# Kernel optimization log

Measured on AMD Instinct MI355X. Metric: run time of the kernel, lower is better.

The kernel has to match this reference:

```python
import jax, jax.numpy as jnp
import numpy as np

D_MODEL = 1024
N_HEADS = 16
D_K = D_MODEL // N_HEADS


def setup_inputs() -> dict:
    key = jax.random.key(0)
    ks = jax.random.split(key, 12)
    B, S, D = 4, 2048, D_MODEL
    scale = 1.0 / np.sqrt(D)
    inp = {
        'query': jax.random.normal(ks[0], (B, S, D), jnp.float32),
        'key': jax.random.normal(ks[1], (B, S, D), jnp.float32),
        'value': jax.random.normal(ks[2], (B, S, D), jnp.float32),
        'Wq': jax.random.normal(ks[3], (D, D), jnp.float32) * scale,
        'bq': jax.random.normal(ks[4], (D,), jnp.float32) * 0.02,
        'Wk': jax.random.normal(ks[5], (D, D), jnp.float32) * scale,
        'bk': jax.random.normal(ks[6], (D,), jnp.float32) * 0.02,
        'Wv': jax.random.normal(ks[7], (D, D), jnp.float32) * scale,
        'bv': jax.random.normal(ks[8], (D,), jnp.float32) * 0.02,
        'Wo': jax.random.normal(ks[9], (D, D), jnp.float32) * scale,
        'bo': jax.random.normal(ks[10], (D,), jnp.float32) * 0.02,
    }
    return inp


def reference(query, key, value, Wq, bq, Wk, bk, Wv, bv, Wo, bo):
    B, S, D = query.shape
    # torch nn.Linear: y = x @ W^T + b
    def proj(x, W, b):
        y = jnp.einsum('bsd,ed->bse', x, W) + b
        # [B,S,D] -> [B,H,S,d_k]
        return y.reshape(B, S, N_HEADS, D_K).transpose(0, 2, 1, 3)

    q = proj(query, Wq, bq)
    k = proj(key, Wk, bk)
    v = proj(value, Wv, bv)

    scores = jnp.einsum('bhqd,bhkd->bhqk', q, k) / jnp.sqrt(jnp.float32(D_K))
    attn = jax.nn.softmax(scores, axis=-1)  # dropout = identity (eval mode)
    out = jnp.einsum('bhqk,bhkd->bhqd', attn, v)
    out = out.transpose(0, 2, 1, 3).reshape(B, S, D)
    return jnp.einsum('bsd,ed->bse', out, Wo) + bo
```

## Files before the change

kernel.cpp:

```cpp
#include <hip/hip_runtime.h>
#include <hip/hip_bf16.h>
#include <cstdint>
#include <cstddef>


#define BATCH   4
#define SEQ     2048
#define D_MODEL 1024
#define NHEADS  16
#define DK      64

typedef __attribute__((ext_vector_type(8))) __bf16 bf16x8_t;
typedef __attribute__((ext_vector_type(4))) float  f32x4;

__device__ inline unsigned int pack2(float lo, float hi) {
  __hip_bfloat162 h = __float22bfloat162_rn(make_float2(lo, hi));
  union { __hip_bfloat162 h; unsigned int u; } c; c.h = h; return c.u;
}
__device__ inline unsigned short f2bf(float f) { return (unsigned short)pack2(f, f); }

#if __has_builtin(__builtin_amdgcn_exp2f)
__device__ inline float fexp2(float x) { return __builtin_amdgcn_exp2f(x); }
#else
__device__ inline float fexp2(float x) { return __expf(x * 0.6931471805599453f); }
#endif

__device__ inline void cvt8(const float* __restrict__ s, unsigned short* __restrict__ d) {
  const float4 a = *(const float4*)s;
  const float4 b = *(const float4*)(s + 4);
  uint4 r;
  r.x = pack2(a.x, a.y); r.y = pack2(a.z, a.w);
  r.z = pack2(b.x, b.y); r.w = pack2(b.z, b.w);
  *(uint4*)d = r;
}

typedef __attribute__((address_space(3))) unsigned int lds_u32_t;
typedef const __attribute__((address_space(1))) unsigned int glb_u32_t;
__device__ inline void gld16(const unsigned short* g, unsigned short* l) {
  __builtin_amdgcn_global_load_lds((glb_u32_t*)(uintptr_t)g,
                                   (lds_u32_t*)(unsigned int)(uintptr_t)l, 16, 0, 0);
}

__global__ __launch_bounds__(256) void cvt3_kernel(
    const float* __restrict__ a, const float* __restrict__ b, const float* __restrict__ c,
    unsigned short* __restrict__ oa, unsigned short* __restrict__ ob, unsigned short* __restrict__ oc)
{
  const float* s = (blockIdx.y == 0) ? a : (blockIdx.y == 1) ? b : c;
  unsigned short* d = (blockIdx.y == 0) ? oa : (blockIdx.y == 1) ? ob : oc;
  const size_t i = ((size_t)blockIdx.x * 256 + threadIdx.x) * 8;
  cvt8(s + i, d + i);
}
__global__ __launch_bounds__(256) void cvt4_kernel(
    const float* __restrict__ a, const float* __restrict__ b,
    const float* __restrict__ c, const float* __restrict__ dd,
    unsigned short* __restrict__ oa, unsigned short* __restrict__ ob,
    unsigned short* __restrict__ oc, unsigned short* __restrict__ od)
{
  const float* s = (blockIdx.y == 0) ? a : (blockIdx.y == 1) ? b : (blockIdx.y == 2) ? c : dd;
  unsigned short* d = (blockIdx.y == 0) ? oa : (blockIdx.y == 1) ? ob : (blockIdx.y == 2) ? oc : od;
  const size_t i = ((size_t)blockIdx.x * 256 + threadIdx.x) * 8;
  cvt8(s + i, d + i);
}

__device__ inline void gemm_core(const unsigned short* __restrict__ A,
                                 const unsigned short* __restrict__ W,
                                 unsigned short* a_lds, unsigned short* b_lds,
                                 int m0, int n0, f32x4 (&acc)[4][4])
{
  const int tid  = threadIdx.x;
  const int lane = tid & 63;
  const int wv   = tid >> 6;
  const int l15  = lane & 15;
  const int quad = lane >> 4;
  const int wm = (wv & 1) * 64;
  const int wn = (wv >> 1) * 64;

  const int srow = tid >> 2;
  const int sch  = (tid & 3) ^ (srow & 3);
  const unsigned short* Ap0 = A + (size_t)(m0 + srow) * D_MODEL + sch * 8;
  const unsigned short* Ap1 = Ap0 + (size_t)64 * D_MODEL;
  const unsigned short* Wp0 = W + (size_t)(n0 + srow) * D_MODEL + sch * 8;
  const unsigned short* Wp1 = Wp0 + (size_t)64 * D_MODEL;
  unsigned short* al0 = a_lds + wv * 512;
  unsigned short* al1 = a_lds + 2048 + wv * 512;
  unsigned short* bl0 = b_lds + wv * 512;
  unsigned short* bl1 = b_lds + 2048 + wv * 512;

  const int pq = (quad ^ (l15 & 3)) * 8;

  for (int k0 = 0; k0 < D_MODEL; k0 += 32) {
    __syncthreads();
    gld16(Ap0 + k0, al0);
    gld16(Ap1 + k0, al1);
    gld16(Wp0 + k0, bl0);
    gld16(Wp1 + k0, bl1);
    __syncthreads();

    bf16x8_t af[4], bfr[4];
#pragma unroll
    for (int i = 0; i < 4; ++i)
      af[i] = *(const bf16x8_t*)&a_lds[(wm + i * 16 + l15) * 32 + pq];
#pragma unroll
    for (int j = 0; j < 4; ++j)
      bfr[j] = *(const bf16x8_t*)&b_lds[(wn + j * 16 + l15) * 32 + pq];

#pragma unroll
    for (int i = 0; i < 4; ++i)
#pragma unroll
      for (int j = 0; j < 4; ++j)
        acc[i][j] = __builtin_amdgcn_mfma_f32_16x16x32_bf16(af[i], bfr[j], acc[i][j], 0, 0, 0);
  }
}

__global__ __launch_bounds__(256) void qkv_kernel(
    const unsigned short* __restrict__ qb, const unsigned short* __restrict__ kb,
    const unsigned short* __restrict__ vb,
    const unsigned short* __restrict__ wq, const unsigned short* __restrict__ wk,
    const unsigned short* __restrict__ wvp,
    const float* __restrict__ bq, const float* __restrict__ bk, const float* __restrict__ bv,
    unsigned short* __restrict__ Qws, unsigned short* __restrict__ Kws,
    unsigned short* __restrict__ Vws)
{
  __shared__ unsigned short a_lds[128 * 32];
  __shared__ unsigned short b_lds[128 * 32];

  const int z = blockIdx.z;
  const unsigned short* A = (z == 0) ? qb : (z == 1) ? kb : vb;
  const unsigned short* W = (z == 0) ? wq : (z == 1) ? wk : wvp;
  const float* bias       = (z == 0) ? bq : (z == 1) ? bk : bv;
  unsigned short* C       = (z == 0) ? Qws : (z == 1) ? Kws : Vws;
  const int m0 = blockIdx.x * 128;
  const int n0 = blockIdx.y * 128;

  f32x4 acc[4][4];
#pragma unroll
  for (int i = 0; i < 4; ++i)
#pragma unroll
    for (int j = 0; j < 4; ++j)
      acc[i][j] = (f32x4){0.f, 0.f, 0.f, 0.f};

  gemm_core(A, W, a_lds, b_lds, m0, n0, acc);

  const int tid  = threadIdx.x;
  const int lane = tid & 63;
  const int wv   = tid >> 6;
  const int l15  = lane & 15;
  const int quad = lane >> 4;
  const int wm = (wv & 1) * 64;
  const int wn = (wv >> 1) * 64;
  if (z == 2) {
    for (int j = 0; j < 4; ++j) {
      const int n = n0 + wn + j * 16 + l15;
      const int hh = n >> 6, dd = n & 63;
      const float bvl = bias[n];
      for (int i = 0; i < 4; ++i) {
        const int mbase = m0 + wm + i * 16 + quad * 4;
        const int bb = mbase >> 11, ss = mbase & 2047;
        uint2 w2 = make_uint2(pack2(acc[i][j][0] + bvl, acc[i][j][1] + bvl),
                              pack2(acc[i][j][2] + bvl, acc[i][j][3] + bvl));
        *(uint2*)(C + (((size_t)bb * NHEADS + hh) * DK + dd) * SEQ + ss) = w2;
      }
    }
  } else {
    const float oscale = (z == 0) ? 0.18033688011112042f : 1.0f;
    for (int j = 0; j < 4; ++j) {
      const int n = n0 + wn + j * 16 + l15;
      const int hh = n >> 6, dd = n & 63;
      const float bvl = bias[n];
      for (int i = 0; i < 4; ++i) {
        const int mbase = m0 + wm + i * 16 + quad * 4;
        const int bb = mbase >> 11, ss = mbase & 2047;
        unsigned short* dst = C + (((size_t)bb * NHEADS + hh) * SEQ + ss) * DK + dd;
        for (int r = 0; r < 4; ++r)
          dst[(size_t)r * DK] = f2bf((acc[i][j][r] + bvl) * oscale);
      }
    }
  }
}

__global__ __launch_bounds__(256) void outproj_kernel(
    const unsigned short* __restrict__ A, const unsigned short* __restrict__ W,
    const float* __restrict__ bias, float* __restrict__ C)
{
  __shared__ unsigned short a_lds[128 * 32];
  __shared__ unsigned short b_lds[128 * 32];
  const int m0 = blockIdx.x * 128;
  const int n0 = blockIdx.y * 128;

  f32x4 acc[4][4];
#pragma unroll
  for (int i = 0; i < 4; ++i)
#pragma unroll
    for (int j = 0; j < 4; ++j)
      acc[i][j] = (f32x4){0.f, 0.f, 0.f, 0.f};

  gemm_core(A, W, a_lds, b_lds, m0, n0, acc);

  const int tid  = threadIdx.x;
  const int lane = tid & 63;
  const int wv   = tid >> 6;
  const int l15  = lane & 15;
  const int quad = lane >> 4;
  const int wm = (wv & 1) * 64;
  const int wn = (wv >> 1) * 64;
  for (int j = 0; j < 4; ++j) {
    const int n = n0 + wn + j * 16 + l15;
    const float bvl = bias[n];
    for (int i = 0; i < 4; ++i) {
      const int mbase = m0 + wm + i * 16 + quad * 4;
      for (int r = 0; r < 4; ++r)
        C[(size_t)(mbase + r) * D_MODEL + n] = acc[i][j][r] + bvl;
    }
  }
}

__global__ __launch_bounds__(512, 6) void attn_kernel(
    const unsigned short* __restrict__ Q,
    const unsigned short* __restrict__ K,
    const unsigned short* __restrict__ Vt,
    unsigned short* __restrict__ Oattn)
{
  __shared__ unsigned short k_sw[2 * 64 * 64];
  __shared__ unsigned short vt_sw[2 * 64 * 64];

  const int tid  = threadIdx.x;
  const int lane = tid & 63;
  const int wv   = tid >> 6;
  const int l15  = lane & 15;
  const int quad = lane >> 4;
  const int bh   = blockIdx.x;
  const int q0   = blockIdx.y * 128;
  const size_t hoff = (size_t)bh * SEQ * DK;
  const unsigned short* Qh  = Q  + hoff;
  const unsigned short* Kh  = K  + hoff;
  const unsigned short* Vth = Vt + hoff;

  bf16x8_t qf0, qf1;
  {
    const unsigned short* qr = Qh + (size_t)(q0 + wv * 16 + l15) * DK;
    qf0 = *(const bf16x8_t*)(qr + quad * 8);
    qf1 = *(const bf16x8_t*)(qr + 32 + quad * 8);
  }

  f32x4 o[4];
#pragma unroll
  for (int t = 0; t < 4; ++t) o[t] = (f32x4){0.f, 0.f, 0.f, 0.f};
  float mval = -1e30f, lval = 0.f;

  const int sr  = lane >> 3;
  const int pc  = lane & 7;
  const int row = wv * 8 + sr;
  const int sem = pc ^ sr ^ wv;
  const unsigned short* KsA = Kh  + (size_t)row * DK  + sem * 8;
  const unsigned short* VsA = Vth + (size_t)row * SEQ + sem * 8;
  unsigned short* kd = k_sw  + wv * 512;
  unsigned short* vd = vt_sw + wv * 512;

#define STAGE(buf, key0) do {                                        \
    gld16(KsA + (size_t)(key0) * DK, kd + (buf) * 4096);             \
    gld16(VsA + (key0),              vd + (buf) * 4096);             \
  } while (0)

  const int srcA = l15 + ((quad & 1) << 5);
  const int srcB = srcA + 16;
  const int hi   = quad >> 1;

  STAGE(0, 0);
  __syncthreads();

  int cur = 0;
  for (int kb = 0; kb < SEQ / 64; ++kb) {
    if (kb + 1 < SEQ / 64) STAGE(cur ^ 1, (kb + 1) * 64);

    const unsigned short* kcur = k_sw  + cur * 4096;
    const unsigned short* vcur = vt_sw + cur * 4096;

    f32x4 s[4];
    __builtin_amdgcn_s_setprio(1);
#pragma unroll
    for (int t = 0; t < 4; ++t) {
      const int r = t * 16 + l15;
      const int sw = (r & 7) ^ (r >> 3);
      bf16x8_t kf0 = *(const bf16x8_t*)&kcur[r * 64 + ((quad ^ sw) << 3)];
      bf16x8_t kf1 = *(const bf16x8_t*)&kcur[r * 64 + (((quad | 4) ^ sw) << 3)];
      f32x4 z = (f32x4){0.f, 0.f, 0.f, 0.f};
      z = __builtin_amdgcn_mfma_f32_16x16x32_bf16(kf0, qf0, z, 0, 0, 0);
      z = __builtin_amdgcn_mfma_f32_16x16x32_bf16(kf1, qf1, z, 0, 0, 0);
      s[t] = z;
    }
    __builtin_amdgcn_s_setprio(0);

    float mx = s[0][0];
#pragma unroll
    for (int t = 0; t < 4; ++t)
#pragma unroll
      for (int r = 0; r < 4; ++r) mx = fmaxf(mx, s[t][r]);
    mx = fmaxf(mx, __shfl_xor(mx, 16));
    mx = fmaxf(mx, __shfl_xor(mx, 32));
    if (__any(mx > mval + 8.0f)) {
      const float mnew  = fmaxf(mval, mx);
      const float alpha = fexp2(mval - mnew);
      mval = mnew;
      lval *= alpha;
#pragma unroll
      for (int t = 0; t < 4; ++t) o[t] *= alpha;
    }
    float rs = 0.f;
    unsigned int u[4][2];
#pragma unroll
    for (int t = 0; t < 4; ++t) {
      const float p0 = fexp2(s[t][0] - mval);
      const float p1 = fexp2(s[t][1] - mval);
      const float p2 = fexp2(s[t][2] - mval);
      const float p3 = fexp2(s[t][3] - mval);
      rs += (p0 + p1) + (p2 + p3);
      u[t][0] = pack2(p0, p1);
      u[t][1] = pack2(p2, p3);
    }
    rs += __shfl_xor(rs, 16);
    rs += __shfl_xor(rs, 32);
    lval += rs;

    unsigned int w0[4], w1[4];
#pragma unroll
    for (int c = 0; c < 2; ++c) {
      unsigned int* wc = c ? w1 : w0;
      const unsigned int uA0 = u[2 * c][0],     uA1 = u[2 * c][1];
      const unsigned int uB0 = u[2 * c + 1][0], uB1 = u[2 * c + 1][1];
      unsigned int a, b;
      a = (unsigned int)__shfl((int)uA0, srcA); b = (unsigned int)__shfl((int)uB0, srcA);
      wc[0] = hi ? b : a;
      a = (unsigned int)__shfl((int)uA1, srcA); b = (unsigned int)__shfl((int)uB1, srcA);
      wc[1] = hi ? b : a;
      a = (unsigned int)__shfl((int)uA0, srcB); b = (unsigned int)__shfl((int)uB0, srcB);
      wc[2] = hi ? b : a;
      a = (unsigned int)__shfl((int)uA1, srcB); b = (unsigned int)__shfl((int)uB1, srcB);
      wc[3] = hi ? b : a;
    }
    union Cv { unsigned int w[4]; bf16x8_t v; };
    Cv cv0, cv1;
    cv0.w[0] = w0[0]; cv0.w[1] = w0[1]; cv0.w[2] = w0[2]; cv0.w[3] = w0[3];
    cv1.w[0] = w1[0]; cv1.w[1] = w1[1]; cv1.w[2] = w1[2]; cv1.w[3] = w1[3];
    const bf16x8_t pf0 = cv0.v;
    const bf16x8_t pf1 = cv1.v;

    __builtin_amdgcn_s_setprio(1);
#pragma unroll
    for (int nt = 0; nt < 4; ++nt) {
      const int r = nt * 16 + l15;
      const int sw = (r & 7) ^ (r >> 3);
      bf16x8_t vf0 = *(const bf16x8_t*)&vcur[r * 64 + ((quad ^ sw) << 3)];
      bf16x8_t vf1 = *(const bf16x8_t*)&vcur[r * 64 + (((quad | 4) ^ sw) << 3)];
      o[nt] = __builtin_amdgcn_mfma_f32_16x16x32_bf16(vf0, pf0, o[nt], 0, 0, 0);
      o[nt] = __builtin_amdgcn_mfma_f32_16x16x32_bf16(vf1, pf1, o[nt], 0, 0, 0);
    }
    __builtin_amdgcn_s_setprio(0);

    __syncthreads();
    cur ^= 1;
  }
#undef STAGE

  const int bb = bh >> 4, hh = bh & 15;
  const float inv = 1.0f / lval;
  unsigned short* orow = Oattn + (size_t)(bb * SEQ + q0 + wv * 16 + l15) * D_MODEL + hh * DK + quad * 4;
#pragma unroll
  for (int nt = 0; nt < 4; ++nt) {
    f32x4 v = o[nt];
    *(uint2*)(orow + nt * 16) = make_uint2(pack2(v[0] * inv, v[1] * inv),
                                           pack2(v[2] * inv, v[3] * inv));
  }
}

extern "C" void kernel_launch(void* const* d_in, const int* in_sizes, int n_in,
                              void* d_out, int out_size, void* d_ws, size_t ws_size,
                              hipStream_t stream) {
  const float* query = (const float*)d_in[0];
  const float* key   = (const float*)d_in[1];
  const float* value = (const float*)d_in[2];
  const float* Wq    = (const float*)d_in[3];
  const float* bq    = (const float*)d_in[4];
  const float* Wk    = (const float*)d_in[5];
  const float* bk    = (const float*)d_in[6];
  const float* Wv    = (const float*)d_in[7];
  const float* bv    = (const float*)d_in[8];
  const float* Wo    = (const float*)d_in[9];
  const float* bo    = (const float*)d_in[10];

  const size_t E  = (size_t)BATCH * SEQ * D_MODEL;
  const size_t WE = (size_t)D_MODEL * D_MODEL;
  unsigned short* ws  = (unsigned short*)d_ws;
  unsigned short* Qws = ws;
  unsigned short* Kws = ws + E;
  unsigned short* Vws = ws + 2 * E;
  unsigned short* qb  = ws + 3 * E;
  unsigned short* kb  = ws + 4 * E;
  unsigned short* vb  = ws + 5 * E;
  unsigned short* wqb = ws + 6 * E;
  unsigned short* wkb = wqb + WE;
  unsigned short* wvb = wqb + 2 * WE;
  unsigned short* wob = wqb + 3 * WE;
  unsigned short* Aws = qb;

  cvt3_kernel<<<dim3(E / 2048, 3), 256, 0, stream>>>(query, key, value, qb, kb, vb);
  cvt4_kernel<<<dim3(WE / 2048, 4), 256, 0, stream>>>(Wq, Wk, Wv, Wo, wqb, wkb, wvb, wob);

  qkv_kernel<<<dim3(BATCH * SEQ / 128, D_MODEL / 128, 3), 256, 0, stream>>>(
      qb, kb, vb, wqb, wkb, wvb, bq, bk, bv, Qws, Kws, Vws);
  attn_kernel<<<dim3(BATCH * NHEADS, SEQ / 128), 512, 0, stream>>>(Qws, Kws, Vws, Aws);
  outproj_kernel<<<dim3(BATCH * SEQ / 128, D_MODEL / 128), 256, 0, stream>>>(
      Aws, wob, bo, (float*)d_out);
}
```

Before: 402.5 us.

## Process two query tiles per attention block to reuse K/V staging

Each attention block now handles 256 query rows instead of 128: every wave keeps two independent Q fragments, accumulators and softmax states, and reuses each K/V tile loaded into shared memory for both. This halves the K/V global loads and LDS fragment reads per query row. The cost is higher register pressure (launch bounds lowered from 6 to 4 waves per SIMD) and half as many blocks in the grid (512), which may reduce occupancy and the ability to hide latency.

```diff
diff --git a/kernel.cpp b/kernel.cpp
--- a/kernel.cpp
+++ b/kernel.cpp
@@ -214,7 +214,34 @@
   }
 }
 
-__global__ __launch_bounds__(512, 6) void attn_kernel(
+__device__ inline void exchP(const unsigned int (&u)[4][2], int srcA, int srcB, int hi,
+                             bf16x8_t& pf0, bf16x8_t& pf1)
+{
+  unsigned int w0[4], w1[4];
+#pragma unroll
+  for (int c = 0; c < 2; ++c) {
+    unsigned int* wc = c ? w1 : w0;
+    const unsigned int uA0 = u[2 * c][0],     uA1 = u[2 * c][1];
+    const unsigned int uB0 = u[2 * c + 1][0], uB1 = u[2 * c + 1][1];
+    unsigned int a, b;
+    a = (unsigned int)__shfl((int)uA0, srcA); b = (unsigned int)__shfl((int)uB0, srcA);
+    wc[0] = hi ? b : a;
+    a = (unsigned int)__shfl((int)uA1, srcA); b = (unsigned int)__shfl((int)uB1, srcA);
+    wc[1] = hi ? b : a;
+    a = (unsigned int)__shfl((int)uA0, srcB); b = (unsigned int)__shfl((int)uB0, srcB);
+    wc[2] = hi ? b : a;
+    a = (unsigned int)__shfl((int)uA1, srcB); b = (unsigned int)__shfl((int)uB1, srcB);
+    wc[3] = hi ? b : a;
+  }
+  union Cv { unsigned int w[4]; bf16x8_t v; };
+  Cv cv0, cv1;
+  cv0.w[0] = w0[0]; cv0.w[1] = w0[1]; cv0.w[2] = w0[2]; cv0.w[3] = w0[3];
+  cv1.w[0] = w1[0]; cv1.w[1] = w1[1]; cv1.w[2] = w1[2]; cv1.w[3] = w1[3];
+  pf0 = cv0.v;
+  pf1 = cv1.v;
+}
+
+__global__ __launch_bounds__(512, 4) void attn_kernel(
     const unsigned short* __restrict__ Q,
     const unsigned short* __restrict__ K,
     const unsigned short* __restrict__ Vt,
@@ -229,23 +256,30 @@
   const int l15  = lane & 15;
   const int quad = lane >> 4;
   const int bh   = blockIdx.x;
-  const int q0   = blockIdx.y * 128;
+  const int q0   = blockIdx.y * 256;
   const size_t hoff = (size_t)bh * SEQ * DK;
   const unsigned short* Qh  = Q  + hoff;
   const unsigned short* Kh  = K  + hoff;
   const unsigned short* Vth = Vt + hoff;
 
-  bf16x8_t qf0, qf1;
+  bf16x8_t qfA0, qfA1, qfB0, qfB1;
   {
-    const unsigned short* qr = Qh + (size_t)(q0 + wv * 16 + l15) * DK;
-    qf0 = *(const bf16x8_t*)(qr + quad * 8);
-    qf1 = *(const bf16x8_t*)(qr + 32 + quad * 8);
-  }
-
-  f32x4 o[4];
-#pragma unroll
-  for (int t = 0; t < 4; ++t) o[t] = (f32x4){0.f, 0.f, 0.f, 0.f};
-  float mval = -1e30f, lval = 0.f;
+    const unsigned short* qrA = Qh + (size_t)(q0 + wv * 16 + l15) * DK;
+    const unsigned short* qrB = qrA + (size_t)128 * DK;
+    qfA0 = *(const bf16x8_t*)(qrA + quad * 8);
+    qfA1 = *(const bf16x8_t*)(qrA + 32 + quad * 8);
+    qfB0 = *(const bf16x8_t*)(qrB + quad * 8);
+    qfB1 = *(const bf16x8_t*)(qrB + 32 + quad * 8);
+  }
+
+  f32x4 oA[4], oB[4];
+#pragma unroll
+  for (int t = 0; t < 4; ++t) {
+    oA[t] = (f32x4){0.f, 0.f, 0.f, 0.f};
+    oB[t] = (f32x4){0.f, 0.f, 0.f, 0.f};
+  }
+  float mA = -1e30f, lA = 0.f;
+  float mB = -1e30f, lB = 0.f;
 
   const int sr  = lane >> 3;
   const int pc  = lane & 7;
@@ -275,7 +309,7 @@
     const unsigned short* kcur = k_sw  + cur * 4096;
     const unsigned short* vcur = vt_sw + cur * 4096;
 
-    f32x4 s[4];
+    f32x4 sA[4], sB[4];
     __builtin_amdgcn_s_setprio(1);
 #pragma unroll
     for (int t = 0; t < 4; ++t) {
@@ -283,66 +317,84 @@
       const int sw = (r & 7) ^ (r >> 3);
       bf16x8_t kf0 = *(const bf16x8_t*)&kcur[r * 64 + ((quad ^ sw) << 3)];
       bf16x8_t kf1 = *(const bf16x8_t*)&kcur[r * 64 + (((quad | 4) ^ sw) << 3)];
-      f32x4 z = (f32x4){0.f, 0.f, 0.f, 0.f};
-      z = __builtin_amdgcn_mfma_f32_16x16x32_bf16(kf0, qf0, z, 0, 0, 0);
-      z = __builtin_amdgcn_mfma_f32_16x16x32_bf16(kf1, qf1, z, 0, 0, 0);
-      s[t] = z;
+      f32x4 zA = (f32x4){0.f, 0.f, 0.f, 0.f};
+      zA = __builtin_amdgcn_mfma_f32_16x16x32_bf16(kf0, qfA0, zA, 0, 0, 0);
+      zA = __builtin_amdgcn_mfma_f32_16x16x32_bf16(kf1, qfA1, zA, 0, 0, 0);
+      sA[t] = zA;
+      f32x4 zB = (f32x4){0.f, 0.f, 0.f, 0.f};
+      zB = __builtin_amdgcn_mfma_f32_16x16x32_bf16(kf0, qfB0, zB, 0, 0, 0);
+      zB = __builtin_amdgcn_mfma_f32_16x16x32_bf16(kf1, qfB1, zB, 0, 0, 0);
+      sB[t] = zB;
     }
     __builtin_amdgcn_s_setprio(0);
 
-    float mx = s[0][0];
-#pragma unroll
-    for (int t = 0; t < 4; ++t)
-#pragma unroll
-      for (int r = 0; r < 4; ++r) mx = fmaxf(mx, s[t][r]);
-    mx = fmaxf(mx, __shfl_xor(mx, 16));
-    mx = fmaxf(mx, __shfl_xor(mx, 32));
-    if (__any(mx > mval + 8.0f)) {
-      const float mnew  = fmaxf(mval, mx);
-      const float alpha = fexp2(mval - mnew);
-      mval = mnew;
-      lval *= alpha;
-#pragma unroll
-      for (int t = 0; t < 4; ++t) o[t] *= alpha;
-    }
-    float rs = 0.f;
-    unsigned int u[4][2];
-#pragma unroll
-    for (int t = 0; t < 4; ++t) {
-      const float p0 = fexp2(s[t][0] - mval);
-      const float p1 = fexp2(s[t][1] - mval);
-      const float p2 = fexp2(s[t][2] - mval);
-      const float p3 = fexp2(s[t][3] - mval);
-      rs += (p0 + p1) + (p2 + p3);
-      u[t][0] = pack2(p0, p1);
-      u[t][1] = pack2(p2, p3);
-    }
-    rs += __shfl_xor(rs, 16);
-    rs += __shfl_xor(rs, 32);
-    lval += rs;
-
-    unsigned int w0[4], w1[4];
-#pragma unroll
-    for (int c = 0; c < 2; ++c) {
-      unsigned int* wc = c ? w1 : w0;
-      const unsigned int uA0 = u[2 * c][0],     uA1 = u[2 * c][1];
-      const unsigned int uB0 = u[2 * c + 1][0], uB1 = u[2 * c + 1][1];
-      unsigned int a, b;
-      a = (unsigned int)__shfl((int)uA0, srcA); b = (unsigned int)__shfl((int)uB0, srcA);
-      wc[0] = hi ? b : a;
-      a = (unsigned int)__shfl((int)uA1, srcA); b = (unsigned int)__shfl((int)uB1, srcA);
-      wc[1] = hi ? b : a;
-      a = (unsigned int)__shfl((int)uA0, srcB); b = (unsigned int)__shfl((int)uB0, srcB);
-      wc[2] = hi ? b : a;
-      a = (unsigned int)__shfl((int)uA1, srcB); b = (unsigned int)__shfl((int)uB1, srcB);
-      wc[3] = hi ? b : a;
-    }
-    union Cv { unsigned int w[4]; bf16x8_t v; };
-    Cv cv0, cv1;
-    cv0.w[0] = w0[0]; cv0.w[1] = w0[1]; cv0.w[2] = w0[2]; cv0.w[3] = w0[3];
-    cv1.w[0] = w1[0]; cv1.w[1] = w1[1]; cv1.w[2] = w1[2]; cv1.w[3] = w1[3];
-    const bf16x8_t pf0 = cv0.v;
-    const bf16x8_t pf1 = cv1.v;
+    bf16x8_t pfA0, pfA1, pfB0, pfB1;
+    {
+      float mx = sA[0][0];
+#pragma unroll
+      for (int t = 0; t < 4; ++t)
+#pragma unroll
+        for (int r = 0; r < 4; ++r) mx = fmaxf(mx, sA[t][r]);
+      mx = fmaxf(mx, __shfl_xor(mx, 16));
+      mx = fmaxf(mx, __shfl_xor(mx, 32));
+      if (__any(mx > mA + 8.0f)) {
+        const float mnew  = fmaxf(mA, mx);
+        const float alpha = fexp2(mA - mnew);
+        mA = mnew;
+        lA *= alpha;
+#pragma unroll
+        for (int t = 0; t < 4; ++t) oA[t] *= alpha;
+      }
+      float rs = 0.f;
+      unsigned int u[4][2];
+#pragma unroll
+      for (int t = 0; t < 4; ++t) {
+        const float p0 = fexp2(sA[t][0] - mA);
+        const float p1 = fexp2(sA[t][1] - mA);
+        const float p2 = fexp2(sA[t][2] - mA);
+        const float p3 = fexp2(sA[t][3] - mA);
+        rs += (p0 + p1) + (p2 + p3);
+        u[t][0] = pack2(p0, p1);
+        u[t][1] = pack2(p2, p3);
+      }
+      rs += __shfl_xor(rs, 16);
+      rs += __shfl_xor(rs, 32);
+      lA += rs;
+      exchP(u, srcA, srcB, hi, pfA0, pfA1);
+    }
+    {
+      float mx = sB[0][0];
+#pragma unroll
+      for (int t = 0; t < 4; ++t)
+#pragma unroll
+        for (int r = 0; r < 4; ++r) mx = fmaxf(mx, sB[t][r]);
+      mx = fmaxf(mx, __shfl_xor(mx, 16));
+      mx = fmaxf(mx, __shfl_xor(mx, 32));
+      if (__any(mx > mB + 8.0f)) {
+        const float mnew  = fmaxf(mB, mx);
+        const float alpha = fexp2(mB - mnew);
+        mB = mnew;
+        lB *= alpha;
+#pragma unroll
+        for (int t = 0; t < 4; ++t) oB[t] *= alpha;
+      }
+      float rs = 0.f;
+      unsigned int u[4][2];
+#pragma unroll
+      for (int t = 0; t < 4; ++t) {
+        const float p0 = fexp2(sB[t][0] - mB);
+        const float p1 = fexp2(sB[t][1] - mB);
+        const float p2 = fexp2(sB[t][2] - mB);
+        const float p3 = fexp2(sB[t][3] - mB);
+        rs += (p0 + p1) + (p2 + p3);
+        u[t][0] = pack2(p0, p1);
+        u[t][1] = pack2(p2, p3);
+      }
+      rs += __shfl_xor(rs, 16);
+      rs += __shfl_xor(rs, 32);
+      lB += rs;
+      exchP(u, srcA, srcB, hi, pfB0, pfB1);
+    }
 
     __builtin_amdgcn_s_setprio(1);
 #pragma unroll
@@ -351,8 +403,10 @@
       const int sw = (r & 7) ^ (r >> 3);
       bf16x8_t vf0 = *(const bf16x8_t*)&vcur[r * 64 + ((quad ^ sw) << 3)];
       bf16x8_t vf1 = *(const bf16x8_t*)&vcur[r * 64 + (((quad | 4) ^ sw) << 3)];
-      o[nt] = __builtin_amdgcn_mfma_f32_16x16x32_bf16(vf0, pf0, o[nt], 0, 0, 0);
-      o[nt] = __builtin_amdgcn_mfma_f32_16x16x32_bf16(vf1, pf1, o[nt], 0, 0, 0);
+      oA[nt] = __builtin_amdgcn_mfma_f32_16x16x32_bf16(vf0, pfA0, oA[nt], 0, 0, 0);
+      oA[nt] = __builtin_amdgcn_mfma_f32_16x16x32_bf16(vf1, pfA1, oA[nt], 0, 0, 0);
+      oB[nt] = __builtin_amdgcn_mfma_f32_16x16x32_bf16(vf0, pfB0, oB[nt], 0, 0, 0);
+      oB[nt] = __builtin_amdgcn_mfma_f32_16x16x32_bf16(vf1, pfB1, oB[nt], 0, 0, 0);
     }
     __builtin_amdgcn_s_setprio(0);
 
@@ -362,13 +416,25 @@
 #undef STAGE
 
   const int bb = bh >> 4, hh = bh & 15;
-  const float inv = 1.0f / lval;
-  unsigned short* orow = Oattn + (size_t)(bb * SEQ + q0 + wv * 16 + l15) * D_MODEL + hh * DK + quad * 4;
-#pragma unroll
-  for (int nt = 0; nt < 4; ++nt) {
-    f32x4 v = o[nt];
-    *(uint2*)(orow + nt * 16) = make_uint2(pack2(v[0] * inv, v[1] * inv),
-                                           pack2(v[2] * inv, v[3] * inv));
+  {
+    const float inv = 1.0f / lA;
+    unsigned short* orow = Oattn + (size_t)(bb * SEQ + q0 + wv * 16 + l15) * D_MODEL + hh * DK + quad * 4;
+#pragma unroll
+    for (int nt = 0; nt < 4; ++nt) {
+      f32x4 v = oA[nt];
+      *(uint2*)(orow + nt * 16) = make_uint2(pack2(v[0] * inv, v[1] * inv),
+                                             pack2(v[2] * inv, v[3] * inv));
+    }
+  }
+  {
+    const float inv = 1.0f / lB;
+    unsigned short* orow = Oattn + (size_t)(bb * SEQ + q0 + 128 + wv * 16 + l15) * D_MODEL + hh * DK + quad * 4;
+#pragma unroll
+    for (int nt = 0; nt < 4; ++nt) {
+      f32x4 v = oB[nt];
+      *(uint2*)(orow + nt * 16) = make_uint2(pack2(v[0] * inv, v[1] * inv),
+                                             pack2(v[2] * inv, v[3] * inv));
+    }
   }
 }
 
@@ -407,7 +473,7 @@
 
   qkv_kernel<<<dim3(BATCH * SEQ / 128, D_MODEL / 128, 3), 256, 0, stream>>>(
       qb, kb, vb, wqb, wkb, wvb, bq, bk, bv, Qws, Kws, Vws);
-  attn_kernel<<<dim3(BATCH * NHEADS, SEQ / 128), 512, 0, stream>>>(Qws, Kws, Vws, Aws);
+  attn_kernel<<<dim3(BATCH * NHEADS, SEQ / 256), 512, 0, stream>>>(Qws, Kws, Vws, Aws);
   outproj_kernel<<<dim3(BATCH * SEQ / 128, D_MODEL / 128), 256, 0, stream>>>(
       Aws, wob, bo, (float*)d_out);
 }
```

After: 375.3 us. 1.07x faster.

## Switch attention to 32x32x16 MFMA with 32 query rows per wave

Applied to the files above, without the earlier changes.

Rewrites the attention inner loop to use 32x32x16 bf16 MFMA tiles, so each wave handles 32 query rows and each block 256, halving the grid's y dimension. The larger tile halves the number of blocks that reload each K/V tile through LDS. It also replaces the cross-lane shuffle that rebuilt the P operand with a single xor-32 exchange. In exchange, register pressure rises, so the launch-bounds occupancy hint drops from 6 to 4 and fewer waves are resident per CU.

```diff
diff --git a/kernel.cpp b/kernel.cpp
--- a/kernel.cpp
+++ b/kernel.cpp
@@ -10,8 +10,9 @@
 #define NHEADS  16
 #define DK      64
 
-typedef __attribute__((ext_vector_type(8))) __bf16 bf16x8_t;
-typedef __attribute__((ext_vector_type(4))) float  f32x4;
+typedef __attribute__((ext_vector_type(8)))  __bf16 bf16x8_t;
+typedef __attribute__((ext_vector_type(4)))  float  f32x4;
+typedef __attribute__((ext_vector_type(16))) float  f32x16;
 
 __device__ inline unsigned int pack2(float lo, float hi) {
   __hip_bfloat162 h = __float22bfloat162_rn(make_float2(lo, hi));
@@ -24,6 +25,10 @@
 #else
 __device__ inline float fexp2(float x) { return __expf(x * 0.6931471805599453f); }
 #endif
+
+__device__ inline unsigned int exch32(unsigned int x) {
+  return (unsigned int)__shfl_xor((int)x, 32);
+}
 
 __device__ inline void cvt8(const float* __restrict__ s, unsigned short* __restrict__ d) {
   const float4 a = *(const float4*)s;
@@ -214,7 +219,7 @@
   }
 }
 
-__global__ __launch_bounds__(512, 6) void attn_kernel(
+__global__ __launch_bounds__(512, 4) void attn_kernel(
     const unsigned short* __restrict__ Q,
     const unsigned short* __restrict__ K,
     const unsigned short* __restrict__ Vt,
@@ -226,25 +231,28 @@
   const int tid  = threadIdx.x;
   const int lane = tid & 63;
   const int wv   = tid >> 6;
-  const int l15  = lane & 15;
-  const int quad = lane >> 4;
+  const int l31  = lane & 31;
+  const int hb   = lane >> 5;
   const int bh   = blockIdx.x;
-  const int q0   = blockIdx.y * 128;
+  const int q0   = blockIdx.y * 256;
   const size_t hoff = (size_t)bh * SEQ * DK;
   const unsigned short* Qh  = Q  + hoff;
   const unsigned short* Kh  = K  + hoff;
   const unsigned short* Vth = Vt + hoff;
 
-  bf16x8_t qf0, qf1;
+  bf16x8_t qf[4];
   {
-    const unsigned short* qr = Qh + (size_t)(q0 + wv * 16 + l15) * DK;
-    qf0 = *(const bf16x8_t*)(qr + quad * 8);
-    qf1 = *(const bf16x8_t*)(qr + 32 + quad * 8);
+    const unsigned short* qr = Qh + (size_t)(q0 + wv * 32 + l31) * DK;
+#pragma unroll
+    for (int kk = 0; kk < 4; ++kk)
+      qf[kk] = *(const bf16x8_t*)(qr + kk * 16 + hb * 8);
   }
 
-  f32x4 o[4];
-#pragma unroll
-  for (int t = 0; t < 4; ++t) o[t] = (f32x4){0.f, 0.f, 0.f, 0.f};
+  f32x16 oAcc[2];
+#pragma unroll
+  for (int dh = 0; dh < 2; ++dh)
+#pragma unroll
+    for (int i = 0; i < 16; ++i) oAcc[dh][i] = 0.f;
   float mval = -1e30f, lval = 0.f;
 
   const int sr  = lane >> 3;
@@ -261,12 +269,11 @@
     gld16(VsA + (key0),              vd + (buf) * 4096);             \
   } while (0)
 
-  const int srcA = l15 + ((quad & 1) << 5);
-  const int srcB = srcA + 16;
-  const int hi   = quad >> 1;
-
   STAGE(0, 0);
   __syncthreads();
+
+  const int swr0 = (l31 & 7) ^ (l31 >> 3);
+  const int swr1 = (l31 & 7) ^ ((l31 >> 3) ^ 4);
 
   int cur = 0;
   for (int kb = 0; kb < SEQ / 64; ++kb) {
@@ -275,27 +282,33 @@
     const unsigned short* kcur = k_sw  + cur * 4096;
     const unsigned short* vcur = vt_sw + cur * 4096;
 
-    f32x4 s[4];
+    f32x16 s0, s1;
+#pragma unroll
+    for (int i = 0; i < 16; ++i) { s0[i] = 0.f; s1[i] = 0.f; }
     __builtin_amdgcn_s_setprio(1);
-#pragma unroll
-    for (int t = 0; t < 4; ++t) {
-      const int r = t * 16 + l15;
-      const int sw = (r & 7) ^ (r >> 3);
-      bf16x8_t kf0 = *(const bf16x8_t*)&kcur[r * 64 + ((quad ^ sw) << 3)];
-      bf16x8_t kf1 = *(const bf16x8_t*)&kcur[r * 64 + (((quad | 4) ^ sw) << 3)];
-      f32x4 z = (f32x4){0.f, 0.f, 0.f, 0.f};
-      z = __builtin_amdgcn_mfma_f32_16x16x32_bf16(kf0, qf0, z, 0, 0, 0);
-      z = __builtin_amdgcn_mfma_f32_16x16x32_bf16(kf1, qf1, z, 0, 0, 0);
-      s[t] = z;
+    {
+      const unsigned short* krow = kcur + l31 * 64;
+#pragma unroll
+      for (int kk = 0; kk < 4; ++kk) {
+        bf16x8_t kf = *(const bf16x8_t*)&krow[((2 * kk + hb) ^ swr0) << 3];
+        s0 = __builtin_amdgcn_mfma_f32_32x32x16_bf16(kf, qf[kk], s0, 0, 0, 0);
+      }
+    }
+    {
+      const unsigned short* krow = kcur + (32 + l31) * 64;
+#pragma unroll
+      for (int kk = 0; kk < 4; ++kk) {
+        bf16x8_t kf = *(const bf16x8_t*)&krow[((2 * kk + hb) ^ swr1) << 3];
+        s1 = __builtin_amdgcn_mfma_f32_32x32x16_bf16(kf, qf[kk], s1, 0, 0, 0);
+      }
     }
     __builtin_amdgcn_s_setprio(0);
 
-    float mx = s[0][0];
-#pragma unroll
-    for (int t = 0; t < 4; ++t)
-#pragma unroll
-      for (int r = 0; r < 4; ++r) mx = fmaxf(mx, s[t][r]);
-    mx = fmaxf(mx, __shfl_xor(mx, 16));
+    float mx = s0[0];
+#pragma unroll
+    for (int i = 1; i < 16; ++i) mx = fmaxf(mx, s0[i]);
+#pragma unroll
+    for (int i = 0; i < 16; ++i) mx = fmaxf(mx, s1[i]);
     mx = fmaxf(mx, __shfl_xor(mx, 32));
     if (__any(mx > mval + 8.0f)) {
       const float mnew  = fmaxf(mval, mx);
@@ -303,56 +316,80 @@
       mval = mnew;
       lval *= alpha;
 #pragma unroll
-      for (int t = 0; t < 4; ++t) o[t] *= alpha;
+      for (int dh = 0; dh < 2; ++dh)
+#pragma unroll
+        for (int i = 0; i < 16; ++i) oAcc[dh][i] *= alpha;
     }
     float rs = 0.f;
-    unsigned int u[4][2];
-#pragma unroll
-    for (int t = 0; t < 4; ++t) {
-      const float p0 = fexp2(s[t][0] - mval);
-      const float p1 = fexp2(s[t][1] - mval);
-      const float p2 = fexp2(s[t][2] - mval);
-      const float p3 = fexp2(s[t][3] - mval);
-      rs += (p0 + p1) + (p2 + p3);
-      u[t][0] = pack2(p0, p1);
-      u[t][1] = pack2(p2, p3);
-    }
-    rs += __shfl_xor(rs, 16);
+    unsigned int w0[8], w1[8];
+#pragma unroll
+    for (int m = 0; m < 8; ++m) {
+      const float p0 = fexp2(s0[2 * m] - mval);
+      const float p1 = fexp2(s0[2 * m + 1] - mval);
+      rs += p0 + p1;
+      w0[m] = pack2(p0, p1);
+    }
+#pragma unroll
+    for (int m = 0; m < 8; ++m) {
+      const float p0 = fexp2(s1[2 * m] - mval);
+      const float p1 = fexp2(s1[2 * m + 1] - mval);
+      rs += p0 + p1;
+      w1[m] = pack2(p0, p1);
+    }
     rs += __shfl_xor(rs, 32);
     lval += rs;
 
-    unsigned int w0[4], w1[4];
-#pragma unroll
-    for (int c = 0; c < 2; ++c) {
-      unsigned int* wc = c ? w1 : w0;
-      const unsigned int uA0 = u[2 * c][0],     uA1 = u[2 * c][1];
-      const unsigned int uB0 = u[2 * c + 1][0], uB1 = u[2 * c + 1][1];
-      unsigned int a, b;
-      a = (unsigned int)__shfl((int)uA0, srcA); b = (unsigned int)__shfl((int)uB0, srcA);
-      wc[0] = hi ? b : a;
-      a = (unsigned int)__shfl((int)uA1, srcA); b = (unsigned int)__shfl((int)uB1, srcA);
-      wc[1] = hi ? b : a;
-      a = (unsigned int)__shfl((int)uA0, srcB); b = (unsigned int)__shfl((int)uB0, srcB);
-      wc[2] = hi ? b : a;
-      a = (unsigned int)__shfl((int)uA1, srcB); b = (unsigned int)__shfl((int)uB1, srcB);
-      wc[3] = hi ? b : a;
-    }
     union Cv { unsigned int w[4]; bf16x8_t v; };
-    Cv cv0, cv1;
-    cv0.w[0] = w0[0]; cv0.w[1] = w0[1]; cv0.w[2] = w0[2]; cv0.w[3] = w0[3];
-    cv1.w[0] = w1[0]; cv1.w[1] = w1[1]; cv1.w[2] = w1[2]; cv1.w[3] = w1[3];
-    const bf16x8_t pf0 = cv0.v;
-    const bf16x8_t pf1 = cv1.v;
+    bf16x8_t pf[4];
+    {
+      const unsigned int e0 = exch32(w0[0]), e1 = exch32(w0[1]);
+      const unsigned int e2 = exch32(w0[2]), e3 = exch32(w0[3]);
+      Cv c;
+      c.w[0] = hb ? e2 : w0[0]; c.w[1] = hb ? e3 : w0[1];
+      c.w[2] = hb ? w0[2] : e0; c.w[3] = hb ? w0[3] : e1;
+      pf[0] = c.v;
+    }
+    {
+      const unsigned int e0 = exch32(w0[4]), e1 = exch32(w0[5]);
+      const unsigned int e2 = exch32(w0[6]), e3 = exch32(w0[7]);
+      Cv c;
+      c.w[0] = hb ? e2 : w0[4]; c.w[1] = hb ? e3 : w0[5];
+      c.w[2] = hb ? w0[6] : e0; c.w[3] = hb ? w0[7] : e1;
+      pf[1] = c.v;
+    }
+    {
+      const unsigned int e0 = exch32(w1[0]), e1 = exch32(w1[1]);
+      const unsigned int e2 = exch32(w1[2]), e3 = exch32(w1[3]);
+      Cv c;
+      c.w[0] = hb ? e2 : w1[0]; c.w[1] = hb ? e3 : w1[1];
+      c.w[2] = hb ? w1[2] : e0; c.w[3] = hb ? w1[3] : e1;
+      pf[2] = c.v;
+    }
+    {
+      const unsigned int e0 = exch32(w1[4]), e1 = exch32(w1[5]);
+      const unsigned int e2 = exch32(w1[6]), e3 = exch32(w1[7]);
+      Cv c;
+      c.w[0] = hb ? e2 : w1[4]; c.w[1] = hb ? e3 : w1[5];
+      c.w[2] = hb ? w1[6] : e0; c.w[3] = hb ? w1[7] : e1;
+      pf[3] = c.v;
+    }
 
     __builtin_amdgcn_s_setprio(1);
-#pragma unroll
-    for (int nt = 0; nt < 4; ++nt) {
-      const int r = nt * 16 + l15;
-      const int sw = (r & 7) ^ (r >> 3);
-      bf16x8_t vf0 = *(const bf16x8_t*)&vcur[r * 64 + ((quad ^ sw) << 3)];
-      bf16x8_t vf1 = *(const bf16x8_t*)&vcur[r * 64 + (((quad | 4) ^ sw) << 3)];
-      o[nt] = __builtin_amdgcn_mfma_f32_16x16x32_bf16(vf0, pf0, o[nt], 0, 0, 0);
-      o[nt] = __builtin_amdgcn_mfma_f32_16x16x32_bf16(vf1, pf1, o[nt], 0, 0, 0);
+    {
+      const unsigned short* vrow = vcur + l31 * 64;
+#pragma unroll
+      for (int t = 0; t < 4; ++t) {
+        bf16x8_t vf = *(const bf16x8_t*)&vrow[((2 * t + hb) ^ swr0) << 3];
+        oAcc[0] = __builtin_amdgcn_mfma_f32_32x32x16_bf16(vf, pf[t], oAcc[0], 0, 0, 0);
+      }
+    }
+    {
+      const unsigned short* vrow = vcur + (32 + l31) * 64;
+#pragma unroll
+      for (int t = 0; t < 4; ++t) {
+        bf16x8_t vf = *(const bf16x8_t*)&vrow[((2 * t + hb) ^ swr1) << 3];
+        oAcc[1] = __builtin_amdgcn_mfma_f32_32x32x16_bf16(vf, pf[t], oAcc[1], 0, 0, 0);
+      }
     }
     __builtin_amdgcn_s_setprio(0);
 
@@ -363,13 +400,18 @@
 
   const int bb = bh >> 4, hh = bh & 15;
   const float inv = 1.0f / lval;
-  unsigned short* orow = Oattn + (size_t)(bb * SEQ + q0 + wv * 16 + l15) * D_MODEL + hh * DK + quad * 4;
-#pragma unroll
-  for (int nt = 0; nt < 4; ++nt) {
-    f32x4 v = o[nt];
-    *(uint2*)(orow + nt * 16) = make_uint2(pack2(v[0] * inv, v[1] * inv),
-                                           pack2(v[2] * inv, v[3] * inv));
-  }
+  unsigned short* orow = Oattn + (size_t)(bb * SEQ + q0 + wv * 32 + l31) * D_MODEL
+                       + hh * DK + hb * 4;
+#pragma unroll
+  for (int dh = 0; dh < 2; ++dh)
+#pragma unroll
+    for (int a = 0; a < 4; ++a) {
+      const float v0 = oAcc[dh][4 * a]     * inv;
+      const float v1 = oAcc[dh][4 * a + 1] * inv;
+      const float v2 = oAcc[dh][4 * a + 2] * inv;
+      const float v3 = oAcc[dh][4 * a + 3] * inv;
+      *(uint2*)(orow + dh * 32 + a * 8) = make_uint2(pack2(v0, v1), pack2(v2, v3));
+    }
 }
 
 extern "C" void kernel_launch(void* const* d_in, const int* in_sizes, int n_in,
@@ -407,7 +449,7 @@
 
   qkv_kernel<<<dim3(BATCH * SEQ / 128, D_MODEL / 128, 3), 256, 0, stream>>>(
       qb, kb, vb, wqb, wkb, wvb, bq, bk, bv, Qws, Kws, Vws);
-  attn_kernel<<<dim3(BATCH * NHEADS, SEQ / 128), 512, 0, stream>>>(Qws, Kws, Vws, Aws);
+  attn_kernel<<<dim3(BATCH * NHEADS, SEQ / 256), 512, 0, stream>>>(Qws, Kws, Vws, Aws);
   outproj_kernel<<<dim3(BATCH * SEQ / 128, D_MODEL / 128), 256, 0, stream>>>(
       Aws, wob, bo, (float*)d_out);
 }
```

Result: faster. 365.4 us (-9.2%).
